# Kernel optimization log

Hardware: AMD Instinct MI355X
Metric: run time of the kernel (lower is better)

## Reference

```python
import jax, jax.numpy as jnp
import numpy as np

ANCHORS = [[(116, 90), (156, 198), (373, 326)],
           [(30, 61), (62, 45), (59, 119)],
           [(10, 13), (16, 30), (33, 23)]]
STRIDES = [32, 16, 8]
NC = 80            # num_classes
SCORE_THRESH = 0.01
NMS_THRESH = 0.45
TOPK = 200
PRE_NMS = 400


def _decode_level(feat, anchors, stride):
    # feat: [B, A*(NC+5), H, W]
    bs, C, H, W = feat.shape
    A = len(anchors)
    p = feat.reshape(bs, A, NC + 5, H, W).transpose(0, 1, 3, 4, 2)  # b a h w c
    gx = jnp.arange(W, dtype=feat.dtype)
    gy = jnp.arange(H, dtype=feat.dtype)
    aw = jnp.asarray([a[0] for a in anchors], feat.dtype)  # anchor w in pixels
    ah = jnp.asarray([a[1] for a in anchors], feat.dtype)
    # (sigmoid(x)+grid)*stride ; exp(w)*(anchor/stride)*stride = exp(w)*anchor
    bx = (jax.nn.sigmoid(p[..., 0]) + gx[None, None, None, :]) * stride
    by = (jax.nn.sigmoid(p[..., 1]) + gy[None, None, :, None]) * stride
    bw = jnp.exp(p[..., 2]) * aw[None, :, None, None]
    bh = jnp.exp(p[..., 3]) * ah[None, :, None, None]
    conf = jax.nn.sigmoid(p[..., 4])
    cls = jax.nn.sigmoid(p[..., 5:])
    out = jnp.concatenate([jnp.stack([bx, by, bw, bh, conf], -1), cls], -1)
    return out.reshape(bs, A * H * W, NC + 5)


def _iou_matrix(boxes):
    # boxes: [K,4] xyxy -> [K,K] IoU
    x1, y1, x2, y2 = boxes[:, 0], boxes[:, 1], boxes[:, 2], boxes[:, 3]
    area = jnp.maximum(x2 - x1, 0.0) * jnp.maximum(y2 - y1, 0.0)
    ix1 = jnp.maximum(x1[:, None], x1[None, :])
    iy1 = jnp.maximum(y1[:, None], y1[None, :])
    ix2 = jnp.minimum(x2[:, None], x2[None, :])
    iy2 = jnp.minimum(y2[:, None], y2[None, :])
    inter = jnp.maximum(ix2 - ix1, 0.0) * jnp.maximum(iy2 - iy1, 0.0)
    union = area[:, None] + area[None, :] - inter
    return inter / jnp.maximum(union, 1e-9)


def _nms_single(pred):
    # pred: [N, 5+NC] with xyxy boxes in cols 0:4, obj conf col 4, class probs 5:
    N = pred.shape[0]
    scores = pred[:, 4:5] * pred[:, 5:]                 # [N, NC]
    flat = scores.reshape(-1)                            # [N*NC]
    flat = jnp.where(flat >= SCORE_THRESH, flat, -1.0)   # low scores sink to bottom
    vals, idx = jax.lax.top_k(flat, PRE_NMS)             # [PRE_NMS]
    box_idx = idx // NC
    cls_idx = idx % NC
    boxes = pred[box_idx, :4]                            # [PRE_NMS, 4]
    valid = vals >= SCORE_THRESH

    iou = _iou_matrix(boxes)
    same_cls = cls_idx[:, None] == cls_idx[None, :]
    later = jnp.arange(PRE_NMS)[None, :] > jnp.arange(PRE_NMS)[:, None]
    sup_mat = (iou > NMS_THRESH) & same_cls & later      # [K,K] i suppresses j

    def body(i, keep):
        sup = sup_mat[i] & keep[i] & valid[i]
        return keep & (~sup)

    keep = jax.lax.fori_loop(0, PRE_NMS, body, jnp.ones(PRE_NMS, bool))
    keep = keep & valid

    final = jnp.where(keep, vals, -1.0)
    sel_scores, sel = jax.lax.top_k(final, TOPK)         # kept boxes, score-sorted
    pad = sel_scores < 0.0
    out_boxes = jnp.where(pad[:, None], 0.0, boxes[sel])
    out_scores = jnp.where(pad, 0.0, sel_scores)
    out_labels = jnp.where(pad, -1.0, cls_idx[sel].astype(pred.dtype))
    return jnp.concatenate([out_boxes, out_scores[:, None], out_labels[:, None]], -1)


def _forward(feat0, feat1, feat2):
    preds = [_decode_level(f, a, s) for f, a, s in
             zip((feat0, feat1, feat2), ANCHORS, STRIDES)]
    pred = jnp.concatenate(preds, axis=1)                # [B, Ntot, 5+NC]
    cx, cy, w, h = pred[..., 0], pred[..., 1], pred[..., 2], pred[..., 3]
    corners = jnp.stack([cx - w / 2, cy - h / 2, cx + w / 2, cy + h / 2], -1)
    pred = jnp.concatenate([corners, pred[..., 4:]], -1)
    return jax.vmap(_nms_single)(pred)                   # [B, TOPK, 6]


def setup_inputs() -> dict:
    key = jax.random.key(0)
    k0, k1, k2 = jax.random.split(key, 3)
    return {
        "feat0": jax.random.normal(k0, (8, 255, 19, 19), jnp.float32),
        "feat1": jax.random.normal(k1, (8, 255, 38, 38), jnp.float32),
        "feat2": jax.random.normal(k2, (8, 255, 76, 76), jnp.float32),
    }


def reference(feat0, feat1, feat2):
    return _forward(feat0, feat1, feat2)
```

## Files before the change

### kernel.cpp

```cpp
#include <hip/hip_runtime.h>
#include <stdint.h>

#define NB      22743
#define L0N     1083
#define L1N     5415
#define PRE     400
#define TOPK_N  200
#define CAP     2048
#define NBATCH  8
#define NBINS   4096
#define MIN_VALID_PFX  ((int)(0xBC23D70Au >> 8))

typedef unsigned long long u64;
typedef unsigned int u32;

__device__ __forceinline__ float sigf(float x) { return 1.0f / (1.0f + expf(-x)); }

__device__ __forceinline__ u32 mono32(float f) {
    u32 u = __float_as_uint(f);
    return (u & 0x80000000u) ? ~u : (u | 0x80000000u);
}
__device__ __forceinline__ float unmono(u32 m) {
    u32 u = (m & 0x80000000u) ? (m & 0x7FFFFFFFu) : ~m;
    return __uint_as_float(u);
}

__device__ __forceinline__ const float* box_base(
    const float* f0, const float* f1, const float* f2,
    int b, int g, int* HW, int* cw, int* ch, float* stride, float* aw, float* ah)
{
    const float* f; int W, off, li;
    if (g < L0N)      { f = f0; W = 19; off = 0;   li = 0; *stride = 32.f; }
    else if (g < L1N) { f = f1; W = 38; off = L0N; li = 1; *stride = 16.f; }
    else              { f = f2; W = 76; off = L1N; li = 2; *stride = 8.f;  }
    const float AWt[3][3] = {{116.f,156.f,373.f},{30.f,62.f,59.f},{10.f,16.f,33.f}};
    const float AHt[3][3] = {{90.f,198.f,326.f},{61.f,45.f,119.f},{13.f,30.f,23.f}};
    int hw = W * W;
    int local = g - off;
    int a = local / hw; int r = local - a * hw;
    int h = r / W; int w = r - h * W;
    *HW = hw; *cw = w; *ch = h;
    *aw = AWt[li][a]; *ah = AHt[li][a];
    return f + (size_t)((b * 255 + a * 85) * hw + h * W + w);
}

template<int MODE>
__global__ void score_pass(const float* __restrict__ f0, const float* __restrict__ f1,
                           const float* __restrict__ f2,
                           u32* __restrict__ ghist, const int2* __restrict__ sel1,
                           const int* __restrict__ t24, u32* __restrict__ cnt,
                           u64* __restrict__ cand)
{
    __shared__ u32 h[NBINS];
    const int b = blockIdx.y;
    if (MODE == 0 || MODE == 1) {
        for (int i = threadIdx.x; i < NBINS; i += blockDim.x) h[i] = 0;
        __syncthreads();
    }
    const int g = blockIdx.x * blockDim.x + threadIdx.x;
    if (g < NB) {
        int HW, cw, ch; float stride, aw, ah;
        const float* p = box_base(f0, f1, f2, b, g, &HW, &cw, &ch, &stride, &aw, &ah);
        float conf = sigf(p[4 * HW]);
        u32 b1 = 0, T = 0;
        if (MODE == 1) b1 = (u32)sel1[b].x;
        if (MODE == 2) T = (u32)t24[b];
        for (int c = 0; c < 80; ++c) {
            float s = conf * sigf(p[(5 + c) * HW]);
            if (s < 0.01f) continue;
            u32 m = mono32(s);
            if (MODE == 0) {
                atomicAdd(&h[m >> 20], 1u);
            } else if (MODE == 1) {
                if ((m >> 20) == b1) atomicAdd(&h[(m >> 8) & 0xFFFu], 1u);
            } else {
                if ((m >> 8) >= T) {
                    u32 pos = atomicAdd(&cnt[b], 1u);
                    if (pos < CAP) {
                        u32 e = (u32)(g * 80 + c);
                        cand[b * CAP + pos] = ((u64)m << 32) | (u64)(0xFFFFFFFFu - e);
                    }
                }
            }
        }
    }
    if (MODE == 0 || MODE == 1) {
        __syncthreads();
        u32* gh = ghist + b * NBINS;
        for (int i = threadIdx.x; i < NBINS; i += blockDim.x)
            if (h[i]) atomicAdd(&gh[i], h[i]);
    }
}

template<int LEVEL>
__global__ __launch_bounds__(256) void scan_k(const u32* __restrict__ ghist,
                                              int2* __restrict__ sel1,
                                              int* __restrict__ t24)
{
    const int b = blockIdx.x;
    const int tid = threadIdx.x;
    const u32* h = ghist + b * NBINS;
    __shared__ u32 lh[NBINS];
    __shared__ u32 part[256];
    __shared__ u32 suf[256];

    const u32 need = (LEVEL == 1) ? (u32)PRE : (u32)(PRE - sel1[b].y);

    for (int i = tid; i < NBINS; i += 256) lh[i] = h[i];
    if (tid == 0) {
        if (LEVEL == 1) sel1[b] = make_int2(0, 0);
        else            t24[b]  = MIN_VALID_PFX;
    }
    __syncthreads();

    u32 ps = 0;
    #pragma unroll
    for (int i = 0; i < 16; ++i) ps += lh[tid * 16 + i];
    part[tid] = ps;
    __syncthreads();

    if (tid == 0) {
        u32 cum = 0;
        for (int t = 255; t >= 0; --t) { suf[t] = cum; cum += part[t]; }
    }
    __syncthreads();

    if (suf[tid] < need && suf[tid] + part[tid] >= need) {
        u32 cum = suf[tid];
        for (int bin = tid * 16 + 15; bin >= tid * 16; --bin) {
            u32 c = lh[bin];
            if (cum + c >= need) {
                if (LEVEL == 1) {
                    sel1[b] = make_int2(bin, (int)cum);
                } else {
                    int t = (sel1[b].x << 12) | bin;
                    t24[b] = (t > MIN_VALID_PFX) ? t : MIN_VALID_PFX;
                }
                break;
            }
            cum += c;
        }
    }
}

__global__ __launch_bounds__(256) void final_k(
    const float* __restrict__ f0, const float* __restrict__ f1, const float* __restrict__ f2,
    const u32* __restrict__ cnt, const u64* __restrict__ cand, float* __restrict__ out)
{
    __shared__ u64 keys[CAP];
    __shared__ u64 SKEY[PRE];
    __shared__ float X1[PRE], Y1[PRE], X2[PRE], Y2[PRE], VAL[PRE];
    __shared__ int CLS[PRE];
    __shared__ u64 SUP[PRE][8];
    __shared__ u64 VBM[8];
    __shared__ u64 KBM[8];

    const int b = blockIdx.x;
    const int tid = threadIdx.x;
    const int n = (int)min(cnt[b], (u32)CAP);

    for (int i = tid; i < n; i += 256) keys[i] = cand[b * CAP + i];
    for (int i = tid; i < PRE; i += 256) SKEY[i] = 0ull;
    if (tid < 8) { VBM[tid] = 0ull; KBM[tid] = 0ull; }
    __syncthreads();

    for (int e = tid; e < n; e += 256) {
        u64 my = keys[e];
        int r = 0;
        for (int k = 0; k < n; ++k) r += (keys[k] > my);
        if (r < PRE) SKEY[r] = my;
    }
    __syncthreads();

    #pragma unroll
    for (int rr = 0; rr < 2; ++rr) {
        int i = rr * 256 + tid;
        bool valid = false;
        if (i < PRE) {
            u64 kk = SKEY[i];
            float v; int g, c;
            if (kk == 0ull) { v = -1.0f; g = 0; c = 0; }
            else {
                u32 m = (u32)(kk >> 32);
                u32 e = 0xFFFFFFFFu - (u32)(kk & 0xFFFFFFFFu);
                v = unmono(m);
                g = (int)(e / 80u);
                c = (int)(e - (u32)g * 80u);
                valid = true;
            }
            VAL[i] = v; CLS[i] = c;
            int HW, cw, ch; float stride, aw, ah;
            const float* p = box_base(f0, f1, f2, b, g, &HW, &cw, &ch, &stride, &aw, &ah);
            float cx = (sigf(p[0])      + (float)cw) * stride;
            float cy = (sigf(p[HW])     + (float)ch) * stride;
            float bw = expf(p[2 * HW]) * aw;
            float bh = expf(p[3 * HW]) * ah;
            X1[i] = cx - bw * 0.5f; Y1[i] = cy - bh * 0.5f;
            X2[i] = cx + bw * 0.5f; Y2[i] = cy + bh * 0.5f;
        }
        u64 bal = __ballot(valid);
        if ((tid & 63) == 0) VBM[rr * 4 + (tid >> 6)] = bal;
    }
    __syncthreads();

    for (int t = tid; t < PRE * 8; t += 256) {
        int i = t >> 3, w = t & 7;
        u64 mask = 0ull;
        if (w >= (i >> 6)) {
            float x1i = X1[i], y1i = Y1[i], x2i = X2[i], y2i = Y2[i];
            int ci = CLS[i];
            float ai = fmaxf(x2i - x1i, 0.f) * fmaxf(y2i - y1i, 0.f);
            int jbase = w << 6;
            int j0 = (jbase > i + 1) ? jbase : (i + 1);
            int j1 = (jbase + 64 < PRE) ? (jbase + 64) : PRE;
            for (int j = j0; j < j1; ++j) {
                if (CLS[j] == ci) {
                    float ix1 = fmaxf(x1i, X1[j]);
                    float iy1 = fmaxf(y1i, Y1[j]);
                    float ix2 = fminf(x2i, X2[j]);
                    float iy2 = fminf(y2i, Y2[j]);
                    float inter = fmaxf(ix2 - ix1, 0.f) * fmaxf(iy2 - iy1, 0.f);
                    float aj = fmaxf(X2[j] - X1[j], 0.f) * fmaxf(Y2[j] - Y1[j], 0.f);
                    float iou = inter / fmaxf(ai + aj - inter, 1e-9f);
                    if (iou > 0.45f) mask |= 1ull << (j - jbase);
                }
            }
        }
        SUP[i][w] = mask;
    }
    __syncthreads();

    if (tid == 0) {
        u64 kp[7], A[7], B[7];
        #pragma unroll
        for (int w = 0; w < 7; ++w) kp[w] = VBM[w];
        #pragma unroll
        for (int w = 0; w < 7; ++w) A[w] = SUP[0][w];
        #pragma unroll
        for (int w = 0; w < 7; ++w) B[w] = SUP[1][w];
        #pragma unroll
        for (int w = 0; w < 7; ++w) {
            const int base = w << 6;
            const int lim = (w == 6) ? 16 : 64;
            for (int bi = 0; bi < lim; bi += 2) {
                int i = base + bi;
                if ((kp[w] >> bi) & 1) {
                    #pragma unroll
                    for (int w2 = 0; w2 < 7; ++w2) kp[w2] &= ~A[w2];
                }
                int ip2 = (i + 2 < PRE) ? (i + 2) : (PRE - 1);
                #pragma unroll
                for (int w2 = 0; w2 < 7; ++w2) A[w2] = SUP[ip2][w2];
                if ((kp[w] >> (bi + 1)) & 1) {
                    #pragma unroll
                    for (int w2 = 0; w2 < 7; ++w2) kp[w2] &= ~B[w2];
                }
                int ip3 = (i + 3 < PRE) ? (i + 3) : (PRE - 1);
                #pragma unroll
                for (int w2 = 0; w2 < 7; ++w2) B[w2] = SUP[ip3][w2];
            }
        }
        #pragma unroll
        for (int w = 0; w < 7; ++w) KBM[w] = kp[w];
    }
    __syncthreads();

    int totk = 0;
    #pragma unroll
    for (int w = 0; w < 7; ++w) totk += __popcll(KBM[w]);
    for (int j = tid; j < PRE; j += 256) {
        int w = j >> 6, bi = j & 63;
        int pre_kept = 0;
        for (int ww = 0; ww < w; ++ww) pre_kept += __popcll(KBM[ww]);
        u64 kw = KBM[w];
        pre_kept += __popcll(kw & ((1ull << bi) - 1ull));
        bool kept = (kw >> bi) & 1;
        int slot = kept ? pre_kept : (totk + j - pre_kept);
        if (slot < TOPK_N) {
            float* o = out + ((size_t)b * TOPK_N + slot) * 6;
            if (kept) {
                o[0] = X1[j]; o[1] = Y1[j]; o[2] = X2[j]; o[3] = Y2[j];
                o[4] = VAL[j]; o[5] = (float)CLS[j];
            } else {
                o[0] = 0.f; o[1] = 0.f; o[2] = 0.f; o[3] = 0.f; o[4] = 0.f; o[5] = -1.f;
            }
        }
    }
}

extern "C" void kernel_launch(void* const* d_in, const int* in_sizes, int n_in,
                              void* d_out, int out_size, void* d_ws, size_t ws_size,
                              hipStream_t stream)
{
    const float* f0 = (const float*)d_in[0];
    const float* f1 = (const float*)d_in[1];
    const float* f2 = (const float*)d_in[2];
    float* out = (float*)d_out;
    char* ws = (char*)d_ws;

    u32*  ghist1 = (u32*)(ws);
    u32*  ghist2 = (u32*)(ws + 131072);
    u32*  cnt    = (u32*)(ws + 262144);
    int2* sel1   = (int2*)(ws + 262176);
    int*  t24    = (int*)(ws + 262240);
    u64*  cand   = (u64*)(ws + 262272);

    hipMemsetAsync(ws, 0, 262176, stream);

    dim3 grid((NB + 255) / 256, NBATCH);
    score_pass<0><<<grid, 256, 0, stream>>>(f0, f1, f2, ghist1, sel1, t24, cnt, cand);
    scan_k<1><<<NBATCH, 256, 0, stream>>>(ghist1, sel1, t24);
    score_pass<1><<<grid, 256, 0, stream>>>(f0, f1, f2, ghist2, sel1, t24, cnt, cand);
    scan_k<2><<<NBATCH, 256, 0, stream>>>(ghist2, sel1, t24);
    score_pass<2><<<grid, 256, 0, stream>>>(f0, f1, f2, ghist1, sel1, t24, cnt, cand);
    final_k<<<NBATCH, 256, 0, stream>>>(f0, f1, f2, cnt, cand, out);
}
```

Measured before the change: 378.7 us.

## Split final NMS into sort, suppression and output kernels; prune boxes by conf

```diff
diff --git a/kernel.cpp b/kernel.cpp
--- a/kernel.cpp
+++ b/kernel.cpp
@@ -8,8 +8,9 @@
 #define TOPK_N  200
 #define CAP     2048
 #define NBATCH  8
-#define NBINS   4096
-#define MIN_VALID_PFX  ((int)(0xBC23D70Au >> 8))
+#define NBINS1  2048
+#define NBINS2  4096
+#define MIN_VALID_P9 (0xBC23D70Au >> 9)
 
 typedef unsigned long long u64;
 typedef unsigned int u32;
@@ -48,46 +49,60 @@
 __global__ void score_pass(const float* __restrict__ f0, const float* __restrict__ f1,
                            const float* __restrict__ f2,
                            u32* __restrict__ ghist, const int2* __restrict__ sel1,
-                           const int* __restrict__ t24, u32* __restrict__ cnt,
+                           const u32* __restrict__ t23, u32* __restrict__ cnt,
                            u64* __restrict__ cand)
 {
-    __shared__ u32 h[NBINS];
+    __shared__ u32 h[(MODE == 0) ? NBINS1 * 4 : ((MODE == 1) ? NBINS2 : 1)];
     const int b = blockIdx.y;
-    if (MODE == 0 || MODE == 1) {
-        for (int i = threadIdx.x; i < NBINS; i += blockDim.x) h[i] = 0;
-        __syncthreads();
-    }
-    const int g = blockIdx.x * blockDim.x + threadIdx.x;
+    const int tid = threadIdx.x;
+    if (MODE == 0) { for (int i = tid; i < NBINS1 * 4; i += 256) h[i] = 0; __syncthreads(); }
+    if (MODE == 1) { for (int i = tid; i < NBINS2; i += 256) h[i] = 0; __syncthreads(); }
+
+    const int g = blockIdx.x * blockDim.x + tid;
     if (g < NB) {
         int HW, cw, ch; float stride, aw, ah;
         const float* p = box_base(f0, f1, f2, b, g, &HW, &cw, &ch, &stride, &aw, &ah);
         float conf = sigf(p[4 * HW]);
         u32 b1 = 0, T = 0;
         if (MODE == 1) b1 = (u32)sel1[b].x;
-        if (MODE == 2) T = (u32)t24[b];
-        for (int c = 0; c < 80; ++c) {
-            float s = conf * sigf(p[(5 + c) * HW]);
-            if (s < 0.01f) continue;
-            u32 m = mono32(s);
-            if (MODE == 0) {
-                atomicAdd(&h[m >> 20], 1u);
-            } else if (MODE == 1) {
-                if ((m >> 20) == b1) atomicAdd(&h[(m >> 8) & 0xFFFu], 1u);
-            } else {
-                if ((m >> 8) >= T) {
-                    u32 pos = atomicAdd(&cnt[b], 1u);
-                    if (pos < CAP) {
-                        u32 e = (u32)(g * 80 + c);
-                        cand[b * CAP + pos] = ((u64)m << 32) | (u64)(0xFFFFFFFFu - e);
+        if (MODE == 2) T = t23[b];
+        bool do_box;
+        if (MODE == 0)      do_box = (conf >= 0.01f);
+        else if (MODE == 1) do_box = ((mono32(conf) >> 21) >= b1);
+        else                do_box = ((mono32(conf) >> 9)  >= T);
+        if (do_box) {
+            for (int c = 0; c < 80; ++c) {
+                float s = conf * sigf(p[(5 + c) * HW]);
+                if (s < 0.01f) continue;
+                u32 m = mono32(s);
+                if (MODE == 0) {
+                    atomicAdd(&h[(m >> 21) * 4 + (tid & 3)], 1u);
+                } else if (MODE == 1) {
+                    if ((m >> 21) == b1) atomicAdd(&h[(m >> 9) & 0xFFFu], 1u);
+                } else {
+                    if ((m >> 9) >= T) {
+                        u32 pos = atomicAdd(&cnt[b], 1u);
+                        if (pos < CAP) {
+                            u32 e = (u32)(g * 80 + c);
+                            cand[b * CAP + pos] = ((u64)m << 32) | (u64)(0xFFFFFFFFu - e);
+                        }
                     }
                 }
             }
         }
     }
-    if (MODE == 0 || MODE == 1) {
+    if (MODE == 0) {
         __syncthreads();
-        u32* gh = ghist + b * NBINS;
-        for (int i = threadIdx.x; i < NBINS; i += blockDim.x)
+        u32* gh = ghist + b * NBINS1;
+        for (int i = tid; i < NBINS1; i += 256) {
+            u32 s = h[i*4] + h[i*4+1] + h[i*4+2] + h[i*4+3];
+            if (s) atomicAdd(&gh[i], s);
+        }
+    }
+    if (MODE == 1) {
+        __syncthreads();
+        u32* gh = ghist + b * NBINS2;
+        for (int i = tid; i < NBINS2; i += 256)
             if (h[i]) atomicAdd(&gh[i], h[i]);
     }
 }
@@ -95,27 +110,29 @@
 template<int LEVEL>
 __global__ __launch_bounds__(256) void scan_k(const u32* __restrict__ ghist,
                                               int2* __restrict__ sel1,
-                                              int* __restrict__ t24)
-{
+                                              u32* __restrict__ t23)
+{
+    constexpr int NB_ = (LEVEL == 1) ? NBINS1 : NBINS2;
+    constexpr int CH  = NB_ / 256;
     const int b = blockIdx.x;
     const int tid = threadIdx.x;
-    const u32* h = ghist + b * NBINS;
-    __shared__ u32 lh[NBINS];
+    const u32* h = ghist + b * NB_;
+    __shared__ u32 lh[NB_];
     __shared__ u32 part[256];
     __shared__ u32 suf[256];
 
     const u32 need = (LEVEL == 1) ? (u32)PRE : (u32)(PRE - sel1[b].y);
 
-    for (int i = tid; i < NBINS; i += 256) lh[i] = h[i];
+    for (int i = tid; i < NB_; i += 256) lh[i] = h[i];
     if (tid == 0) {
         if (LEVEL == 1) sel1[b] = make_int2(0, 0);
-        else            t24[b]  = MIN_VALID_PFX;
+        else            t23[b]  = MIN_VALID_P9;
     }
     __syncthreads();
 
     u32 ps = 0;
     #pragma unroll
-    for (int i = 0; i < 16; ++i) ps += lh[tid * 16 + i];
+    for (int i = 0; i < CH; ++i) ps += lh[tid * CH + i];
     part[tid] = ps;
     __syncthreads();
 
@@ -127,14 +144,14 @@
 
     if (suf[tid] < need && suf[tid] + part[tid] >= need) {
         u32 cum = suf[tid];
-        for (int bin = tid * 16 + 15; bin >= tid * 16; --bin) {
+        for (int bin = tid * CH + CH - 1; bin >= tid * CH; --bin) {
             u32 c = lh[bin];
             if (cum + c >= need) {
                 if (LEVEL == 1) {
                     sel1[b] = make_int2(bin, (int)cum);
                 } else {
-                    int t = (sel1[b].x << 12) | bin;
-                    t24[b] = (t > MIN_VALID_PFX) ? t : MIN_VALID_PFX;
+                    u32 t = ((u32)sel1[b].x << 12) | (u32)bin;
+                    t23[b] = (t > MIN_VALID_P9) ? t : MIN_VALID_P9;
                 }
                 break;
             }
@@ -143,91 +160,112 @@
     }
 }
 
-__global__ __launch_bounds__(256) void final_k(
+__global__ __launch_bounds__(512) void sortdec_k(
     const float* __restrict__ f0, const float* __restrict__ f1, const float* __restrict__ f2,
-    const u32* __restrict__ cnt, const u64* __restrict__ cand, float* __restrict__ out)
+    const u32* __restrict__ cnt, const u64* __restrict__ cand,
+    float4* __restrict__ DB, float* __restrict__ VALG, int* __restrict__ CLSG,
+    u64* __restrict__ VBMG)
 {
     __shared__ u64 keys[CAP];
     __shared__ u64 SKEY[PRE];
-    __shared__ float X1[PRE], Y1[PRE], X2[PRE], Y2[PRE], VAL[PRE];
-    __shared__ int CLS[PRE];
-    __shared__ u64 SUP[PRE][8];
+    const int b = blockIdx.x;
+    const int tid = threadIdx.x;
+    const int n = (int)min(cnt[b], (u32)CAP);
+
+    for (int i = tid; i < n; i += 512) keys[i] = cand[b * CAP + i];
+    for (int i = tid; i < PRE; i += 512) SKEY[i] = 0ull;
+    __syncthreads();
+
+    for (int e = tid; e < n; e += 512) {
+        u64 my = keys[e];
+        int r = 0, k = 0;
+        for (; k + 4 <= n; k += 4)
+            r += (int)(keys[k] > my) + (int)(keys[k+1] > my)
+               + (int)(keys[k+2] > my) + (int)(keys[k+3] > my);
+        for (; k < n; ++k) r += (int)(keys[k] > my);
+        if (r < PRE) SKEY[r] = my;
+    }
+    __syncthreads();
+
+    const int i = tid;
+    bool valid = false;
+    if (i < PRE) {
+        u64 kk = SKEY[i];
+        float v; int g, c;
+        if (kk) {
+            u32 m = (u32)(kk >> 32);
+            u32 e = 0xFFFFFFFFu - (u32)(kk & 0xFFFFFFFFu);
+            v = unmono(m); g = (int)(e / 80u); c = (int)(e - (u32)g * 80u);
+            valid = true;
+        } else { v = -1.0f; g = 0; c = 0; }
+        int HW, cw, ch; float stride, aw, ah;
+        const float* p = box_base(f0, f1, f2, b, g, &HW, &cw, &ch, &stride, &aw, &ah);
+        float cx = (sigf(p[0])  + (float)cw) * stride;
+        float cy = (sigf(p[HW]) + (float)ch) * stride;
+        float bw = expf(p[2 * HW]) * aw;
+        float bh = expf(p[3 * HW]) * ah;
+        DB[b * PRE + i] = make_float4(cx - bw * 0.5f, cy - bh * 0.5f,
+                                      cx + bw * 0.5f, cy + bh * 0.5f);
+        VALG[b * PRE + i] = v;
+        CLSG[b * PRE + i] = c;
+    }
+    u64 bal = __ballot(valid);
+    if ((tid & 63) == 0 && (tid >> 6) < 7) VBMG[b * 8 + (tid >> 6)] = bal;
+}
+
+__global__ __launch_bounds__(256) void sup_k(const float4* __restrict__ DB,
+                                             const int* __restrict__ CLSG,
+                                             u64* __restrict__ SUPG)
+{
+    __shared__ float4 BX[PRE];
+    __shared__ int LC[PRE];
+    const int w = blockIdx.x, b = blockIdx.y;
+    const int tid = threadIdx.x;
+    for (int i = tid; i < PRE; i += 256) { BX[i] = DB[b * PRE + i]; LC[i] = CLSG[b * PRE + i]; }
+    __syncthreads();
+
+    const int jbase = w << 6;
+    const int j1 = (jbase + 64 < PRE) ? (jbase + 64) : PRE;
+    for (int i = tid; i < PRE; i += 256) {
+        u64 mask = 0ull;
+        if (w >= (i >> 6)) {
+            float4 bi = BX[i]; int ci = LC[i];
+            float ai = fmaxf(bi.z - bi.x, 0.f) * fmaxf(bi.w - bi.y, 0.f);
+            for (int j = jbase; j < j1; ++j) {
+                float4 bj = BX[j];
+                bool ok = (LC[j] == ci) && (j > i);
+                float ix1 = fmaxf(bi.x, bj.x), iy1 = fmaxf(bi.y, bj.y);
+                float ix2 = fminf(bi.z, bj.z), iy2 = fminf(bi.w, bj.w);
+                float inter = fmaxf(ix2 - ix1, 0.f) * fmaxf(iy2 - iy1, 0.f);
+                float aj = fmaxf(bj.z - bj.x, 0.f) * fmaxf(bj.w - bj.y, 0.f);
+                float iou = inter / fmaxf(ai + aj - inter, 1e-9f);
+                if (ok && iou > 0.45f) mask |= 1ull << (j - jbase);
+            }
+        }
+        SUPG[(b * PRE + i) * 7 + w] = mask;
+    }
+}
+
+__global__ __launch_bounds__(256) void nms_out_k(
+    const u64* __restrict__ SUPG, const u64* __restrict__ VBMG,
+    const float4* __restrict__ DB, const float* __restrict__ VALG,
+    const int* __restrict__ CLSG, float* __restrict__ out)
+{
+    __shared__ u64 SUP[PRE][7];
+    __shared__ float4 BX[PRE];
+    __shared__ float VALs[PRE];
+    __shared__ int LC[PRE];
     __shared__ u64 VBM[8];
     __shared__ u64 KBM[8];
 
     const int b = blockIdx.x;
     const int tid = threadIdx.x;
-    const int n = (int)min(cnt[b], (u32)CAP);
-
-    for (int i = tid; i < n; i += 256) keys[i] = cand[b * CAP + i];
-    for (int i = tid; i < PRE; i += 256) SKEY[i] = 0ull;
-    if (tid < 8) { VBM[tid] = 0ull; KBM[tid] = 0ull; }
-    __syncthreads();
-
-    for (int e = tid; e < n; e += 256) {
-        u64 my = keys[e];
-        int r = 0;
-        for (int k = 0; k < n; ++k) r += (keys[k] > my);
-        if (r < PRE) SKEY[r] = my;
-    }
-    __syncthreads();
-
-    #pragma unroll
-    for (int rr = 0; rr < 2; ++rr) {
-        int i = rr * 256 + tid;
-        bool valid = false;
-        if (i < PRE) {
-            u64 kk = SKEY[i];
-            float v; int g, c;
-            if (kk == 0ull) { v = -1.0f; g = 0; c = 0; }
-            else {
-                u32 m = (u32)(kk >> 32);
-                u32 e = 0xFFFFFFFFu - (u32)(kk & 0xFFFFFFFFu);
-                v = unmono(m);
-                g = (int)(e / 80u);
-                c = (int)(e - (u32)g * 80u);
-                valid = true;
-            }
-            VAL[i] = v; CLS[i] = c;
-            int HW, cw, ch; float stride, aw, ah;
-            const float* p = box_base(f0, f1, f2, b, g, &HW, &cw, &ch, &stride, &aw, &ah);
-            float cx = (sigf(p[0])      + (float)cw) * stride;
-            float cy = (sigf(p[HW])     + (float)ch) * stride;
-            float bw = expf(p[2 * HW]) * aw;
-            float bh = expf(p[3 * HW]) * ah;
-            X1[i] = cx - bw * 0.5f; Y1[i] = cy - bh * 0.5f;
-            X2[i] = cx + bw * 0.5f; Y2[i] = cy + bh * 0.5f;
-        }
-        u64 bal = __ballot(valid);
-        if ((tid & 63) == 0) VBM[rr * 4 + (tid >> 6)] = bal;
-    }
-    __syncthreads();
-
-    for (int t = tid; t < PRE * 8; t += 256) {
-        int i = t >> 3, w = t & 7;
-        u64 mask = 0ull;
-        if (w >= (i >> 6)) {
-            float x1i = X1[i], y1i = Y1[i], x2i = X2[i], y2i = Y2[i];
-            int ci = CLS[i];
-            float ai = fmaxf(x2i - x1i, 0.f) * fmaxf(y2i - y1i, 0.f);
-            int jbase = w << 6;
-            int j0 = (jbase > i + 1) ? jbase : (i + 1);
-            int j1 = (jbase + 64 < PRE) ? (jbase + 64) : PRE;
-            for (int j = j0; j < j1; ++j) {
-                if (CLS[j] == ci) {
-                    float ix1 = fmaxf(x1i, X1[j]);
-                    float iy1 = fmaxf(y1i, Y1[j]);
-                    float ix2 = fminf(x2i, X2[j]);
-                    float iy2 = fminf(y2i, Y2[j]);
-                    float inter = fmaxf(ix2 - ix1, 0.f) * fmaxf(iy2 - iy1, 0.f);
-                    float aj = fmaxf(X2[j] - X1[j], 0.f) * fmaxf(Y2[j] - Y1[j], 0.f);
-                    float iou = inter / fmaxf(ai + aj - inter, 1e-9f);
-                    if (iou > 0.45f) mask |= 1ull << (j - jbase);
-                }
-            }
-        }
-        SUP[i][w] = mask;
-    }
+
+    for (int t = tid; t < PRE * 7; t += 256) ((u64*)SUP)[t] = SUPG[b * PRE * 7 + t];
+    for (int i = tid; i < PRE; i += 256) {
+        BX[i] = DB[b * PRE + i]; VALs[i] = VALG[b * PRE + i]; LC[i] = CLSG[b * PRE + i];
+    }
+    if (tid < 8) { VBM[tid] = (tid < 7) ? VBMG[b * 8 + tid] : 0ull; KBM[tid] = 0ull; }
     __syncthreads();
 
     if (tid == 0) {
@@ -279,8 +317,9 @@
         if (slot < TOPK_N) {
             float* o = out + ((size_t)b * TOPK_N + slot) * 6;
             if (kept) {
-                o[0] = X1[j]; o[1] = Y1[j]; o[2] = X2[j]; o[3] = Y2[j];
-                o[4] = VAL[j]; o[5] = (float)CLS[j];
+                float4 bx = BX[j];
+                o[0] = bx.x; o[1] = bx.y; o[2] = bx.z; o[3] = bx.w;
+                o[4] = VALs[j]; o[5] = (float)LC[j];
             } else {
                 o[0] = 0.f; o[1] = 0.f; o[2] = 0.f; o[3] = 0.f; o[4] = 0.f; o[5] = -1.f;
             }
@@ -298,20 +337,27 @@
     float* out = (float*)d_out;
     char* ws = (char*)d_ws;
 
-    u32*  ghist1 = (u32*)(ws);
-    u32*  ghist2 = (u32*)(ws + 131072);
-    u32*  cnt    = (u32*)(ws + 262144);
-    int2* sel1   = (int2*)(ws + 262176);
-    int*  t24    = (int*)(ws + 262240);
-    u64*  cand   = (u64*)(ws + 262272);
-
-    hipMemsetAsync(ws, 0, 262176, stream);
+    u32*    ghist1 = (u32*)(ws);
+    u32*    ghist2 = (u32*)(ws + 65536);
+    u32*    cnt    = (u32*)(ws + 196608);
+    int2*   sel1   = (int2*)(ws + 196640);
+    u32*    t23    = (u32*)(ws + 196704);
+    u64*    VBMG   = (u64*)(ws + 196736);
+    u64*    cand   = (u64*)(ws + 197248);
+    float4* DB     = (float4*)(ws + 328320);
+    float*  VALG   = (float*)(ws + 379520);
+    int*    CLSG   = (int*)(ws + 392320);
+    u64*    SUPG   = (u64*)(ws + 405120);
+
+    hipMemsetAsync(ws, 0, 196640, stream);
 
     dim3 grid((NB + 255) / 256, NBATCH);
-    score_pass<0><<<grid, 256, 0, stream>>>(f0, f1, f2, ghist1, sel1, t24, cnt, cand);
-    scan_k<1><<<NBATCH, 256, 0, stream>>>(ghist1, sel1, t24);
-    score_pass<1><<<grid, 256, 0, stream>>>(f0, f1, f2, ghist2, sel1, t24, cnt, cand);
-    scan_k<2><<<NBATCH, 256, 0, stream>>>(ghist2, sel1, t24);
-    score_pass<2><<<grid, 256, 0, stream>>>(f0, f1, f2, ghist1, sel1, t24, cnt, cand);
-    final_k<<<NBATCH, 256, 0, stream>>>(f0, f1, f2, cnt, cand, out);
-}
+    score_pass<0><<<grid, 256, 0, stream>>>(f0, f1, f2, ghist1, sel1, t23, cnt, cand);
+    scan_k<1><<<NBATCH, 256, 0, stream>>>(ghist1, sel1, t23);
+    score_pass<1><<<grid, 256, 0, stream>>>(f0, f1, f2, ghist2, sel1, t23, cnt, cand);
+    scan_k<2><<<NBATCH, 256, 0, stream>>>(ghist2, sel1, t23);
+    score_pass<2><<<grid, 256, 0, stream>>>(f0, f1, f2, ghist1, sel1, t23, cnt, cand);
+    sortdec_k<<<NBATCH, 512, 0, stream>>>(f0, f1, f2, cnt, cand, DB, VALG, CLSG, VBMG);
+    sup_k<<<dim3(7, NBATCH), 256, 0, stream>>>(DB, CLSG, SUPG);
+    nms_out_k<<<NBATCH, 256, 0, stream>>>(SUPG, VBMG, DB, VALG, CLSG, out);
+}
```

After: 312.3 us. -17.5%, faster.
